# Kernel tuning notes

Measured on AMD Instinct MI355X. Metric: run time of the kernel, lower is better.

## Reference

```python
import jax, jax.numpy as jnp
import numpy as np

# PDELayer config (matches torch defaults)
Nx, Ny = 48, 48
Lx, Ly = 1.0, 1.0
T, dt = 0.01, 0.001
dx, dy = Lx / Nx, Ly / Ny
Nt = int(T / dt)  # 10 sequential stencil steps
B = 16384


def setup_inputs() -> dict:
    key = jax.random.key(0)
    u0 = jax.random.normal(key, (B, 1, Nx, Ny), dtype=jnp.float32)
    alpha_w = jnp.array([0.1, 0.1, 0.1], dtype=jnp.float32)  # alpha_w1..3
    beta_w = jnp.array([0.3, 0.2, 0.2], dtype=jnp.float32)   # beta_w1..3
    return {"u0": u0, "alpha_w": alpha_w, "beta_w": beta_w}


def _coeff_grids(alpha_w, beta_w):
    x = jnp.linspace(0.0, Lx, Nx, dtype=jnp.float32)
    y = jnp.linspace(0.0, Ly, Ny, dtype=jnp.float32)
    yy, xx = jnp.meshgrid(y, x, indexing='ij')  # [Ny, Nx]
    two_pi = jnp.float32(2.0 * np.pi)
    alpha_grid = 0.5 * dt * (alpha_w[0]
                             + alpha_w[1] * jnp.sin(two_pi * yy)
                             + alpha_w[2] * jnp.sin(2.0 * two_pi * yy)) / dx ** 2
    beta_grid = dt * (beta_w[0]
                      + beta_w[1] * jnp.cos(two_pi * xx)
                      + beta_w[2] * jnp.cos(2.0 * two_pi * xx)) / dy ** 2
    return alpha_grid[None], beta_grid[None]  # [1, Nx, Ny] (Nx==Ny)


def reference(u0, alpha_w, beta_w):
    alpha_grid, beta_grid = _coeff_grids(alpha_w, beta_w)
    # reflect-pad once; boundary ring stays frozen during time stepping
    u = jnp.pad(u0[:, 0], ((0, 0), (1, 1), (1, 1)), mode='reflect')  # [B, Nx+2, Ny+2]

    def step(u, _):
        ui = u[:, 1:-1, 1:-1]
        u_xx = u[:, 2:, 1:-1] - 2.0 * ui + u[:, :-2, 1:-1]
        u_yy = u[:, 1:-1, 2:] - 2.0 * ui + u[:, 1:-1, :-2]
        u = u.at[:, 1:-1, 1:-1].set(ui + alpha_grid * u_xx + beta_grid * u_yy)
        return u, None

    u, _ = jax.lax.scan(step, u, None, length=Nt)
    return u[:, 1:-1, 1:-1][:, None]  # [B, 1, Nx, Ny]
```

## Files before the change

kernel.cpp:

```cpp
#include <hip/hip_runtime.h>


typedef float v2f __attribute__((ext_vector_type(2)));

constexpr int NXY   = 48;
constexpr int CELLS = NXY * NXY;
constexpr int NT    = 10;
constexpr int TPB   = 64;

__device__ __forceinline__ float dpp_up(float oldv, float src) {
    return __int_as_float(__builtin_amdgcn_update_dpp(
        __float_as_int(oldv), __float_as_int(src), 0x111, 0xF, 0xF, false));
}
__device__ __forceinline__ float dpp_dn(float oldv, float src) {
    return __int_as_float(__builtin_amdgcn_update_dpp(
        __float_as_int(oldv), __float_as_int(src), 0x101, 0xF, 0xF, false));
}

__global__ __launch_bounds__(TPB)
__attribute__((amdgpu_waves_per_eu(2, 4)))
void pde_heat_kernel(
    const float* __restrict__ u0,
    const float* __restrict__ aw,
    const float* __restrict__ bw,
    float* __restrict__ out)
{
    const int lane = threadIdx.x;
    const int img  = blockIdx.x;
    const int r = lane & 15;
    const int c = lane >> 4;
    const float4* __restrict__ u4 = (const float4*)(u0 + (long long)img * CELLS);
    float4*       __restrict__ o4 = (float4*)(out + (long long)img * CELLS);

    const int fb = r * 36 + c * 3;

    v2f v[3][6], w[3][6];
    #pragma unroll
    for (int ii = 0; ii < 3; ++ii)
        #pragma unroll
        for (int k = 0; k < 3; ++k) {
            float4 t = u4[fb + 12 * ii + k];
            v[ii][2*k]   = (v2f){t.x, t.y};
            v[ii][2*k+1] = (v2f){t.z, t.w};
        }

    const float a0 = aw[0], a1 = aw[1], a2 = aw[2];
    const float b0 = bw[0], b1 = bw[1], b2 = bw[2];
    float ca[3];
    #pragma unroll
    for (int ii = 0; ii < 3; ++ii) {
        float y = (float)(3 * r + ii) * (1.0f / 47.0f);
        ca[ii] = 1.152f * (a0 + a1 * __builtin_amdgcn_sinf(y)
                              + a2 * __builtin_amdgcn_sinf(2.0f * y));
    }
    v2f cb2[6];
    #pragma unroll
    for (int k = 0; k < 6; ++k) {
        float x0 = (float)(12 * c + 2 * k)     * (1.0f / 47.0f);
        float x1 = (float)(12 * c + 2 * k + 1) * (1.0f / 47.0f);
        cb2[k].x = 2.304f * (b0 + b1 * __builtin_amdgcn_cosf(x0)
                                + b2 * __builtin_amdgcn_cosf(2.0f * x0));
        cb2[k].y = 2.304f * (b0 + b1 * __builtin_amdgcn_cosf(x1)
                                + b2 * __builtin_amdgcn_cosf(2.0f * x1));
    }
    v2f cc[3][6];
    #pragma unroll
    for (int ii = 0; ii < 3; ++ii) {
        float t = 1.0f - 2.0f * ca[ii];
        #pragma unroll
        for (int k = 0; k < 6; ++k) {
            cc[ii][k].x = t - 2.0f * cb2[k].x;
            cc[ii][k].y = t - 2.0f * cb2[k].y;
        }
    }

    v2f ab[6], hb[6];
    #pragma unroll
    for (int k = 0; k < 6; ++k) { ab[k] = v[1][k]; hb[k] = v[1][k]; }

    float gH[3];
    #pragma unroll
    for (int ii = 0; ii < 3; ++ii) gH[ii] = (c == 0) ? v[ii][0].y : v[ii][5].x;

    const int laneL = lane - 16, laneR = lane + 16;
    const bool cLft = (c == 0), cRgt = (c == 3);

    #pragma unroll
    for (int k = 0; k < 6; ++k) {
        ab[k].x = dpp_up(ab[k].x, v[2][k].x);
        ab[k].y = dpp_up(ab[k].y, v[2][k].y);
        hb[k].x = dpp_dn(hb[k].x, v[0][k].x);
        hb[k].y = dpp_dn(hb[k].y, v[0][k].y);
    }
    float hlp[3], hrp[3];
    #pragma unroll
    for (int ii = 0; ii < 3; ++ii) {
        hlp[ii] = __shfl(v[ii][5].y, laneL);
        hrp[ii] = __shfl(v[ii][0].x, laneR);
    }

    auto step = [&](const v2f (&src)[3][6], v2f (&dst)[3][6], bool stage) {
        float hl[3], hr[3];
        #pragma unroll
        for (int ii = 0; ii < 3; ++ii) {
            hl[ii] = cLft ? gH[ii] : hlp[ii];
            hr[ii] = cRgt ? gH[ii] : hrp[ii];
        }
        #pragma unroll
        for (int k = 0; k < 6; ++k) {
            v2f cv = src[0][k];
            v2f s1 = ab[k] + src[1][k];
            v2f s2;
            s2.x = ((k > 0) ? src[0][k-1].y : hl[0]) + cv.y;
            s2.y = cv.x + ((k < 5) ? src[0][k+1].x : hr[0]);
            dst[0][k] = cc[0][k] * cv + ca[0] * s1 + cb2[k] * s2;
        }
        #pragma unroll
        for (int k = 0; k < 6; ++k) {
            v2f cv = src[1][k];
            v2f s1 = src[0][k] + src[2][k];
            v2f s2;
            s2.x = ((k > 0) ? src[1][k-1].y : hl[1]) + cv.y;
            s2.y = cv.x + ((k < 5) ? src[1][k+1].x : hr[1]);
            dst[1][k] = cc[1][k] * cv + ca[1] * s1 + cb2[k] * s2;
        }
        #pragma unroll
        for (int k = 0; k < 6; ++k) {
            v2f cv = src[2][k];
            v2f s1 = src[1][k] + hb[k];
            v2f s2;
            s2.x = ((k > 0) ? src[2][k-1].y : hl[2]) + cv.y;
            s2.y = cv.x + ((k < 5) ? src[2][k+1].x : hr[2]);
            dst[2][k] = cc[2][k] * cv + ca[2] * s1 + cb2[k] * s2;
        }
        if (stage) {
            #pragma unroll
            for (int k = 0; k < 6; ++k) {
                ab[k].x = dpp_up(ab[k].x, dst[2][k].x);
                ab[k].y = dpp_up(ab[k].y, dst[2][k].y);
                hb[k].x = dpp_dn(hb[k].x, dst[0][k].x);
                hb[k].y = dpp_dn(hb[k].y, dst[0][k].y);
            }
            #pragma unroll
            for (int ii = 0; ii < 3; ++ii) {
                hlp[ii] = __shfl(dst[ii][5].y, laneL);
                hrp[ii] = __shfl(dst[ii][0].x, laneR);
            }
        }
    };

    #pragma unroll 1
    for (int it = 0; it < NT / 2 - 1; ++it) {
        step(v, w, true);
        step(w, v, true);
    }
    step(v, w, true);
    step(w, v, false);

    #pragma unroll
    for (int ii = 0; ii < 3; ++ii)
        #pragma unroll
        for (int k = 0; k < 3; ++k) {
            float4 t;
            t.x = v[ii][2*k].x;   t.y = v[ii][2*k].y;
            t.z = v[ii][2*k+1].x; t.w = v[ii][2*k+1].y;
            o4[fb + 12 * ii + k] = t;
        }
}

extern "C" void kernel_launch(void* const* d_in, const int* in_sizes, int n_in,
                              void* d_out, int out_size, void* d_ws, size_t ws_size,
                              hipStream_t stream) {
    const float* u0 = (const float*)d_in[0];
    const float* aw = (const float*)d_in[1];
    const float* bw = (const float*)d_in[2];
    float* out = (float*)d_out;

    const int B = in_sizes[0] / CELLS;
    pde_heat_kernel<<<B, TPB, 0, stream>>>(u0, aw, bw, out);
}
```

Before: 75.77 us.

## Process four images per wavefront, reusing coefficients and overlapping load/store with compute

```diff
diff --git a/kernel.cpp b/kernel.cpp
--- a/kernel.cpp
+++ b/kernel.cpp
@@ -7,6 +7,7 @@
 constexpr int CELLS = NXY * NXY;
 constexpr int NT    = 10;
 constexpr int TPB   = 64;
+constexpr int NIMG  = 4;
 
 __device__ __forceinline__ float dpp_up(float oldv, float src) {
     return __int_as_float(__builtin_amdgcn_update_dpp(
@@ -26,23 +27,13 @@
     float* __restrict__ out)
 {
     const int lane = threadIdx.x;
-    const int img  = blockIdx.x;
     const int r = lane & 15;
     const int c = lane >> 4;
-    const float4* __restrict__ u4 = (const float4*)(u0 + (long long)img * CELLS);
-    float4*       __restrict__ o4 = (float4*)(out + (long long)img * CELLS);
+    const long long img0 = (long long)blockIdx.x * NIMG;
+    const float4* __restrict__ u4 = (const float4*)(u0 + img0 * CELLS);
+    float4*       __restrict__ o4 = (float4*)(out + img0 * CELLS);
 
     const int fb = r * 36 + c * 3;
-
-    v2f v[3][6], w[3][6];
-    #pragma unroll
-    for (int ii = 0; ii < 3; ++ii)
-        #pragma unroll
-        for (int k = 0; k < 3; ++k) {
-            float4 t = u4[fb + 12 * ii + k];
-            v[ii][2*k]   = (v2f){t.x, t.y};
-            v[ii][2*k+1] = (v2f){t.z, t.w};
-        }
 
     const float a0 = aw[0], a1 = aw[1], a2 = aw[2];
     const float b0 = bw[0], b1 = bw[1], b2 = bw[2];
@@ -74,32 +65,54 @@
         }
     }
 
+    v2f v[3][6], w[3][6];
     v2f ab[6], hb[6];
-    #pragma unroll
-    for (int k = 0; k < 6; ++k) { ab[k] = v[1][k]; hb[k] = v[1][k]; }
-
-    float gH[3];
-    #pragma unroll
-    for (int ii = 0; ii < 3; ++ii) gH[ii] = (c == 0) ? v[ii][0].y : v[ii][5].x;
+    float gH[3], hlp[3], hrp[3];
 
     const int laneL = lane - 16, laneR = lane + 16;
     const bool cLft = (c == 0), cRgt = (c == 3);
 
-    #pragma unroll
-    for (int k = 0; k < 6; ++k) {
-        ab[k].x = dpp_up(ab[k].x, v[2][k].x);
-        ab[k].y = dpp_up(ab[k].y, v[2][k].y);
-        hb[k].x = dpp_dn(hb[k].x, v[0][k].x);
-        hb[k].y = dpp_dn(hb[k].y, v[0][k].y);
-    }
-    float hlp[3], hrp[3];
-    #pragma unroll
-    for (int ii = 0; ii < 3; ++ii) {
-        hlp[ii] = __shfl(v[ii][5].y, laneL);
-        hrp[ii] = __shfl(v[ii][0].x, laneR);
-    }
-
-    auto step = [&](const v2f (&src)[3][6], v2f (&dst)[3][6], bool stage) {
+    auto load = [&](v2f (&buf)[3][6], int off4) {
+        #pragma unroll
+        for (int ii = 0; ii < 3; ++ii)
+            #pragma unroll
+            for (int k = 0; k < 3; ++k) {
+                float4 t = u4[off4 + 12 * ii + k];
+                buf[ii][2*k]   = (v2f){t.x, t.y};
+                buf[ii][2*k+1] = (v2f){t.z, t.w};
+            }
+    };
+    auto store = [&](const v2f (&buf)[3][6], int off4) {
+        #pragma unroll
+        for (int ii = 0; ii < 3; ++ii)
+            #pragma unroll
+            for (int k = 0; k < 3; ++k) {
+                float4 t;
+                t.x = buf[ii][2*k].x;   t.y = buf[ii][2*k].y;
+                t.z = buf[ii][2*k+1].x; t.w = buf[ii][2*k+1].y;
+                o4[off4 + 12 * ii + k] = t;
+            }
+    };
+    auto prime = [&](const v2f (&buf)[3][6]) {
+        #pragma unroll
+        for (int k = 0; k < 6; ++k) { ab[k] = buf[1][k]; hb[k] = buf[1][k]; }
+        #pragma unroll
+        for (int k = 0; k < 6; ++k) {
+            ab[k].x = dpp_up(ab[k].x, buf[2][k].x);
+            ab[k].y = dpp_up(ab[k].y, buf[2][k].y);
+            hb[k].x = dpp_dn(hb[k].x, buf[0][k].x);
+            hb[k].y = dpp_dn(hb[k].y, buf[0][k].y);
+        }
+        #pragma unroll
+        for (int ii = 0; ii < 3; ++ii)
+            gH[ii] = cLft ? buf[ii][0].y : buf[ii][5].x;
+        #pragma unroll
+        for (int ii = 0; ii < 3; ++ii) {
+            hlp[ii] = __shfl(buf[ii][5].y, laneL);
+            hrp[ii] = __shfl(buf[ii][0].x, laneR);
+        }
+    };
+    auto step = [&](const v2f (&src)[3][6], v2f (&dst)[3][6]) {
         float hl[3], hr[3];
         #pragma unroll
         for (int ii = 0; ii < 3; ++ii) {
@@ -133,39 +146,36 @@
             s2.y = cv.x + ((k < 5) ? src[2][k+1].x : hr[2]);
             dst[2][k] = cc[2][k] * cv + ca[2] * s1 + cb2[k] * s2;
         }
-        if (stage) {
-            #pragma unroll
-            for (int k = 0; k < 6; ++k) {
-                ab[k].x = dpp_up(ab[k].x, dst[2][k].x);
-                ab[k].y = dpp_up(ab[k].y, dst[2][k].y);
-                hb[k].x = dpp_dn(hb[k].x, dst[0][k].x);
-                hb[k].y = dpp_dn(hb[k].y, dst[0][k].y);
-            }
-            #pragma unroll
-            for (int ii = 0; ii < 3; ++ii) {
-                hlp[ii] = __shfl(dst[ii][5].y, laneL);
-                hrp[ii] = __shfl(dst[ii][0].x, laneR);
-            }
+        #pragma unroll
+        for (int k = 0; k < 6; ++k) {
+            ab[k].x = dpp_up(ab[k].x, dst[2][k].x);
+            ab[k].y = dpp_up(ab[k].y, dst[2][k].y);
+            hb[k].x = dpp_dn(hb[k].x, dst[0][k].x);
+            hb[k].y = dpp_dn(hb[k].y, dst[0][k].y);
+        }
+        #pragma unroll
+        for (int ii = 0; ii < 3; ++ii) {
+            hlp[ii] = __shfl(dst[ii][5].y, laneL);
+            hrp[ii] = __shfl(dst[ii][0].x, laneR);
         }
     };
 
+    load(v, fb);
+    prime(v);
     #pragma unroll 1
-    for (int it = 0; it < NT / 2 - 1; ++it) {
-        step(v, w, true);
-        step(w, v, true);
+    for (int p = 0; p < NIMG / 2; ++p) {
+        const int i0 = 2 * p;
+        #pragma unroll 1
+        for (int it = 0; it < NT / 2; ++it) { step(v, w); step(w, v); }
+        load(w, (i0 + 1) * (CELLS / 4) + fb);
+        store(v, i0 * (CELLS / 4) + fb);
+        prime(w);
+        #pragma unroll 1
+        for (int it = 0; it < NT / 2; ++it) { step(w, v); step(v, w); }
+        if (p + 1 < NIMG / 2) load(v, (i0 + 2) * (CELLS / 4) + fb);
+        store(w, (i0 + 1) * (CELLS / 4) + fb);
+        if (p + 1 < NIMG / 2) prime(v);
     }
-    step(v, w, true);
-    step(w, v, false);
-
-    #pragma unroll
-    for (int ii = 0; ii < 3; ++ii)
-        #pragma unroll
-        for (int k = 0; k < 3; ++k) {
-            float4 t;
-            t.x = v[ii][2*k].x;   t.y = v[ii][2*k].y;
-            t.z = v[ii][2*k+1].x; t.w = v[ii][2*k+1].y;
-            o4[fb + 12 * ii + k] = t;
-        }
 }
 
 extern "C" void kernel_launch(void* const* d_in, const int* in_sizes, int n_in,
@@ -177,5 +187,5 @@
     float* out = (float*)d_out;
 
     const int B = in_sizes[0] / CELLS;
-    pde_heat_kernel<<<B, TPB, 0, stream>>>(u0, aw, bw, out);
+    pde_heat_kernel<<<B / NIMG, TPB, 0, stream>>>(u0, aw, bw, out);
 }
```

Result: slower. 81.97 us (+8.2%).
